# Performance work log

Measured on AMD Instinct MI355X. Metric: run time of the kernel, lower is better.

## Reference

```python
import jax, jax.numpy as jnp
import numpy as np

N_NODES = 20000
N_GRAPH = 256
NODE_DIM = 128
MULS = (128, 64, 32)       # node irreps: 128x0e + 64x1o + 32x2e
HC = 32                    # hidden channels per irrep
HIDDEN_DIM = 64
N_PATH = 9                 # feasible uuw paths into 0e+1e+2e
W_NUMEL = N_PATH * HC * HC # 9216


def _tables():
    # real Clebsch-Gordan tensors built from cartesian tensor algebra,
    # normalized so that sum(C**2) = 2*l_out + 1 (component normalization)
    eps = np.zeros((3, 3, 3))
    eps[0, 1, 2] = eps[1, 2, 0] = eps[2, 0, 1] = 1.0
    eps[0, 2, 1] = eps[2, 1, 0] = eps[1, 0, 2] = -1.0
    s2, s6 = 1 / np.sqrt(2), 1 / np.sqrt(6)
    Q2 = np.zeros((5, 3, 3))  # orthonormal basis of traceless symmetric 3x3
    Q2[0, 0, 1] = Q2[0, 1, 0] = s2          # xy
    Q2[1, 1, 2] = Q2[1, 2, 1] = s2          # yz
    Q2[2, 0, 0] = Q2[2, 1, 1] = -s6; Q2[2, 2, 2] = 2 * s6  # z2
    Q2[3, 0, 2] = Q2[3, 2, 0] = s2          # xz
    Q2[4, 0, 0] = s2; Q2[4, 1, 1] = -s2     # x2-y2

    def nrm(C, l3):
        return C * np.sqrt((2 * l3 + 1) / (C ** 2).sum())

    C000 = np.ones((1, 1, 1))
    C022 = np.eye(5)[None, :, :]
    C110 = np.eye(3).reshape(3, 3, 1) / np.sqrt(3)
    C111 = eps / np.sqrt(2)
    C112 = np.transpose(Q2, (1, 2, 0))
    C202 = np.eye(5)[:, None, :]
    C220 = np.eye(5).reshape(5, 5, 1) / np.sqrt(5)
    M = np.einsum('iab,jdb->ijad', Q2, Q2)  # [5,5,3,3]
    C221 = nrm(np.einsum('cad,ijad->ijc', eps, M), 1)
    S = 0.5 * (M + np.transpose(M, (0, 1, 3, 2)))
    S = S - np.trace(S, axis1=2, axis2=3)[..., None, None] * np.eye(3) / 3.0
    C222 = nrm(np.einsum('kad,ijad->ijk', Q2, S), 2)
    # sph2cart change of basis: 9 spherical comps (0e+1e+2e) -> 3x3 cartesian
    Qc = np.zeros((3, 3, 9))
    Qc[:, :, 0] = np.eye(3) / np.sqrt(3)        # isotropic part
    Qc[:, :, 1:4] = eps / np.sqrt(2)            # antisymmetric part
    Qc[:, :, 4:9] = np.transpose(Q2, (1, 2, 0)) # symmetric traceless part
    return [C000, C022, C110, C111, C112, C202, C220, C221, C222], Qc

_CGS, _QC = _tables()


def setup_inputs() -> dict:
    key = jax.random.key(0)
    ks = jax.random.split(key, 12)
    f32 = jnp.float32
    d_sph = MULS[0] + 3 * MULS[1] + 5 * MULS[2]  # 480
    return {
        'x_scalar': jax.random.normal(ks[0], (N_NODES, NODE_DIM), f32),
        'x_spherical': jax.random.normal(ks[1], (N_NODES, d_sph), f32),
        'batch': jnp.sort(jax.random.randint(ks[2], (N_NODES,), 0, N_GRAPH)),
        'W0e': jax.random.normal(ks[3], (MULS[0], HC), f32),
        'W1o': jax.random.normal(ks[4], (MULS[1], HC), f32),
        'W2e': jax.random.normal(ks[5], (MULS[2], HC), f32),
        'Wm1': jax.random.normal(ks[6], (NODE_DIM, HIDDEN_DIM), f32) / np.sqrt(NODE_DIM),
        'bm1': jnp.zeros((HIDDEN_DIM,), f32),
        'Wm2': jax.random.normal(ks[7], (HIDDEN_DIM, W_NUMEL), f32) / np.sqrt(HIDDEN_DIM),
        'bm2': jnp.zeros((W_NUMEL,), f32),
        'P0': jax.random.normal(ks[8], (3 * HC,), f32),
        'P1': jax.random.normal(ks[9], (2 * HC,), f32),
        'P2': jax.random.normal(ks[10], (4 * HC,), f32),
    }


def reference(x_scalar, x_spherical, batch, W0e, W1o, W2e, Wm1, bm1, Wm2, bm2, P0, P1, P2):
    n = x_scalar.shape[0]
    m0, m1, m2 = MULS
    # split node features into irrep blocks
    x0 = x_spherical[:, :m0, None]                        # [N,128,1] 0e
    x1 = x_spherical[:, m0:m0 + 3 * m1].reshape(n, m1, 3) # [N,64,3]  1o
    x2 = x_spherical[:, m0 + 3 * m1:].reshape(n, m2, 5)   # [N,32,5]  2e
    # pre_lin: per-irrep channel mixing (e3nn-style 1/sqrt(fan_in))
    h = [jnp.einsum('num,uv->nvm', x, W) / np.sqrt(W.shape[0])
         for x, W in ((x0, W0e), (x1, W1o), (x2, W2e))]   # each [N,32,2l+1]
    # per-node tensor-product weights from scalar features
    w = (jax.nn.silu(x_scalar @ Wm1 + bm1) @ Wm2 + bm2).reshape(n, N_PATH, HC, HC)
    # uuw tensor product, path order matches _CGS
    paths = ((0, 0), (0, 2), (1, 1), (1, 1), (1, 1), (2, 0), (2, 2), (2, 2), (2, 2))
    inv_u = 1.0 / np.sqrt(HC)
    outs = []
    for k, (i, j) in enumerate(paths):
        C = jnp.asarray(_CGS[k], x_scalar.dtype)
        outs.append(jnp.einsum('pqr,nup,nuq,nuw->nwr', C, h[i], h[j], w[:, k]) * inv_u)
    # post_lin: combine paths of each output l into a single channel
    y0 = jnp.einsum('num,u->nm', jnp.concatenate([outs[0], outs[2], outs[6]], 1), P0) / np.sqrt(3 * HC)
    y1 = jnp.einsum('num,u->nm', jnp.concatenate([outs[3], outs[7]], 1), P1) / np.sqrt(2 * HC)
    y2 = jnp.einsum('num,u->nm', jnp.concatenate([outs[1], outs[4], outs[5], outs[8]], 1), P2) / np.sqrt(4 * HC)
    sph = jnp.concatenate([y0, y1, y2], axis=1)           # [N,9]
    cart = jnp.einsum('abi,ni->nab', jnp.asarray(_QC, sph.dtype), sph)  # [N,3,3]
    red = jax.ops.segment_sum(cart, batch, num_segments=N_GRAPH)        # [B,3,3]
    # if_trace is False (if_iso=False): roll every non-batch dim by 1
    return jnp.roll(jnp.roll(red, 1, axis=1), 1, axis=2)
```

## Files before the change

### kernel.cpp

```cpp
#include <hip/hip_runtime.h>
#include <math.h>

#define OFF_W2P 0
#define OFF_B2P 14336
#define OFF_NRM 14560
#define OFF_V   14592
#define OFF_H0  4494592
#define OFF_H1  5134592
#define OFF_H2  7054592
#define WS_FLOATS 10254592

#define SC_Y0 0.0180421959121758f
#define SC_Y2 0.015625f
#define S2f 0.70710678118654752f
#define S6f 0.40824829046386302f
#define TWOS2f 1.41421356237309505f
#define TWOS6f 0.81649658092772603f
#define ISQRT3 0.57735026918962576f
#define ISQRT5 0.44721359549995794f
#define H0SC 0.08838834764831845f
#define H1SC 0.125f
#define H2SC 0.17677669529663689f

__device__ __constant__ int KARR[7] = {0, 1, 2, 4, 5, 6, 8};

__global__ __launch_bounds__(256) void prep_kernel(
    const float* __restrict__ Wm2, const float* __restrict__ bm2,
    const float* __restrict__ P0, const float* __restrict__ P2,
    float* __restrict__ ws, float* __restrict__ out) {
  int j = blockIdx.x * 256 + threadIdx.x;
  if (j < 2304) out[j] = 0.f;

  if (j < 14336) {
    int s = j >> 11; int rem = j & 2047; int c = rem >> 5; int u = rem & 31;
    int k = KARR[s];
    const float* P;
    float sc;
    switch (s) {
      case 0: P = P0;      sc = SC_Y0; break;
      case 1: P = P2;      sc = SC_Y2; break;
      case 2: P = P0 + 32; sc = SC_Y0; break;
      case 3: P = P2 + 32; sc = SC_Y2; break;
      case 4: P = P2 + 64; sc = SC_Y2; break;
      case 5: P = P0 + 64; sc = SC_Y0; break;
      default: P = P2 + 96; sc = SC_Y2; break;
    }
    const float4* w4 = (const float4*)(Wm2 + c * 9216 + k * 1024 + u * 32);
    const float4* p4 = (const float4*)P;
    float acc = 0.f;
#pragma unroll
    for (int q = 0; q < 8; ++q) {
      float4 a = w4[q], b = p4[q];
      acc += a.x * b.x + a.y * b.y + a.z * b.z + a.w * b.w;
    }
    ws[OFF_W2P + c * 224 + s * 32 + u] = acc * sc;
  } else if (j < 14560) {
    int i = j - 14336; int s = i >> 5; int u = i & 31; int k = KARR[s];
    const float* P;
    float sc;
    switch (s) {
      case 0: P = P0;      sc = SC_Y0; break;
      case 1: P = P2;      sc = SC_Y2; break;
      case 2: P = P0 + 32; sc = SC_Y0; break;
      case 3: P = P2 + 32; sc = SC_Y2; break;
      case 4: P = P2 + 64; sc = SC_Y2; break;
      case 5: P = P0 + 64; sc = SC_Y0; break;
      default: P = P2 + 96; sc = SC_Y2; break;
    }
    const float* b = bm2 + k * 1024 + u * 32;
    float acc = 0.f;
#pragma unroll
    for (int w = 0; w < 32; ++w) acc += b[w] * P[w];
    ws[OFF_B2P + s * 32 + u] = acc * sc;
  } else if (j == 14560) {
    double Q2[5][3][3] = {};
    const double s2d = 0.70710678118654752440, s6d = 0.40824829046386301637;
    Q2[0][0][1] = Q2[0][1][0] = s2d;
    Q2[1][1][2] = Q2[1][2][1] = s2d;
    Q2[2][0][0] = Q2[2][1][1] = -s6d; Q2[2][2][2] = 2.0 * s6d;
    Q2[3][0][2] = Q2[3][2][0] = s2d;
    Q2[4][0][0] = s2d; Q2[4][1][1] = -s2d;
    double ss = 0.0;
    for (int i = 0; i < 5; ++i)
      for (int jj = 0; jj < 5; ++jj) {
        double S[3][3];
        for (int a = 0; a < 3; ++a)
          for (int d = 0; d < 3; ++d) {
            double m1 = 0, m2 = 0;
            for (int b = 0; b < 3; ++b) {
              m1 += Q2[i][a][b] * Q2[jj][d][b];
              m2 += Q2[i][d][b] * Q2[jj][a][b];
            }
            S[a][d] = 0.5 * (m1 + m2);
          }
        double tr = (S[0][0] + S[1][1] + S[2][2]) / 3.0;
        S[0][0] -= tr; S[1][1] -= tr; S[2][2] -= tr;
        for (int kk = 0; kk < 5; ++kk) {
          double cc = 0;
          for (int a = 0; a < 3; ++a)
            for (int d = 0; d < 3; ++d) cc += Q2[kk][a][d] * S[a][d];
          ss += cc * cc;
        }
      }
    ws[OFF_NRM] = (float)sqrt(5.0 / ss);
  }
}

__global__ __launch_bounds__(256) void kb_kernel(
    const float* __restrict__ xs_g, const float* __restrict__ Wm1,
    const float* __restrict__ bm1, const float* __restrict__ ws) {
  __shared__ float xs[64][132];
  __shared__ float hiT[64][64];
  const int n0 = blockIdx.x * 64;
  const int tid = threadIdx.x;

  for (int idx = tid; idx < 2048; idx += 256) {
    int row = idx >> 5, c4 = idx & 31;
    int n = n0 + row;
    float4 v = {0.f, 0.f, 0.f, 0.f};
    if (n < 20000) v = *(const float4*)(xs_g + n * 128 + c4 * 4);
    *(float4*)&xs[row][c4 * 4] = v;
  }
  __syncthreads();

  {
    const int cg = tid & 15, ng = tid >> 4;
    const int c0 = cg * 4, nl = ng * 4;
    float acc[4][4] = {{0.f}};
#pragma unroll 2
    for (int mq = 0; mq < 32; ++mq) {
      float4 xv[4], wv[4];
#pragma unroll
      for (int i = 0; i < 4; ++i) xv[i] = *(float4*)&xs[nl + i][mq * 4];
#pragma unroll
      for (int r = 0; r < 4; ++r) wv[r] = *(const float4*)(Wm1 + (mq * 4 + r) * 64 + c0);
#pragma unroll
      for (int r = 0; r < 4; ++r) {
        const float4 w = wv[r];
#pragma unroll
        for (int i = 0; i < 4; ++i) {
          const float xr = (r == 0) ? xv[i].x : (r == 1) ? xv[i].y : (r == 2) ? xv[i].z : xv[i].w;
          acc[i][0] += xr * w.x; acc[i][1] += xr * w.y;
          acc[i][2] += xr * w.z; acc[i][3] += xr * w.w;
        }
      }
    }
    const float4 bb = *(const float4*)(bm1 + c0);
#pragma unroll
    for (int i = 0; i < 4; ++i) {
#pragma unroll
      for (int jj = 0; jj < 4; ++jj) {
        float z = acc[i][jj] + ((jj == 0) ? bb.x : (jj == 1) ? bb.y : (jj == 2) ? bb.z : bb.w);
        z = z / (1.f + __expf(-z));
        hiT[c0 + jj][nl + i] = z;
      }
    }
  }
  __syncthreads();

  if (tid < 224) {
    const int og = tid >> 3, ng = tid & 7;
    const int o0 = og * 8, nl = ng * 8;
    const float* Wp = ws + OFF_W2P;
    const float4 blo = *(const float4*)(ws + OFF_B2P + o0);
    const float4 bhi = *(const float4*)(ws + OFF_B2P + o0 + 4);
    float acc[8][8];
#pragma unroll
    for (int i = 0; i < 8; ++i) {
      acc[i][0] = blo.x; acc[i][1] = blo.y; acc[i][2] = blo.z; acc[i][3] = blo.w;
      acc[i][4] = bhi.x; acc[i][5] = bhi.y; acc[i][6] = bhi.z; acc[i][7] = bhi.w;
    }
#pragma unroll 2
    for (int c = 0; c < 64; ++c) {
      const float4 hlo = *(float4*)&hiT[c][nl];
      const float4 hhi = *(float4*)&hiT[c][nl + 4];
      const float4 wlo = *(const float4*)(Wp + c * 224 + o0);
      const float4 whi = *(const float4*)(Wp + c * 224 + o0 + 4);
      const float hv[8] = {hlo.x, hlo.y, hlo.z, hlo.w, hhi.x, hhi.y, hhi.z, hhi.w};
      const float wv[8] = {wlo.x, wlo.y, wlo.z, wlo.w, whi.x, whi.y, whi.z, whi.w};
#pragma unroll
      for (int i = 0; i < 8; ++i)
#pragma unroll
        for (int jj = 0; jj < 8; ++jj) acc[i][jj] += hv[i] * wv[jj];
    }
    float* Vout = (float*)(ws + OFF_V);
#pragma unroll
    for (int i = 0; i < 8; ++i) {
      const int n = n0 + nl + i;
      if (n < 20000) {
        float4 a = {acc[i][0], acc[i][1], acc[i][2], acc[i][3]};
        float4 b = {acc[i][4], acc[i][5], acc[i][6], acc[i][7]};
        *(float4*)(Vout + n * 224 + o0) = a;
        *(float4*)(Vout + n * 224 + o0 + 4) = b;
      }
    }
  }
}

__global__ __launch_bounds__(256) void kc_kernel(
    const float* __restrict__ xsph, const float* __restrict__ W0e,
    const float* __restrict__ W1o, const float* __restrict__ W2e,
    float* __restrict__ ws) {
  __shared__ float xp[32][484];
  const int n0 = blockIdx.x * 32;
  const int tid = threadIdx.x;

  for (int idx = tid; idx < 3840; idx += 256) {
    int row = idx / 120, c4 = idx % 120;
    *(float4*)&xp[row][c4 * 4] = *(const float4*)(xsph + (n0 + row) * 480 + c4 * 4);
  }
  __syncthreads();

  if (tid < 64) {
    const int ug = tid & 3, ng = tid >> 2;
    const int u0 = ug * 8;
    float acc[2][8] = {{0.f}};
#pragma unroll 1
    for (int mq = 0; mq < 32; ++mq) {
      float4 xv[2];
      xv[0] = *(float4*)&xp[ng][mq * 4];
      xv[1] = *(float4*)&xp[ng + 16][mq * 4];
      float4 wl[4], wh[4];
#pragma unroll
      for (int r = 0; r < 4; ++r) {
        wl[r] = *(const float4*)(W0e + (mq * 4 + r) * 32 + u0);
        wh[r] = *(const float4*)(W0e + (mq * 4 + r) * 32 + u0 + 4);
      }
#pragma unroll
      for (int r = 0; r < 4; ++r) {
        const float wv[8] = {wl[r].x, wl[r].y, wl[r].z, wl[r].w, wh[r].x, wh[r].y, wh[r].z, wh[r].w};
#pragma unroll
        for (int i = 0; i < 2; ++i) {
          const float xr = (r == 0) ? xv[i].x : (r == 1) ? xv[i].y : (r == 2) ? xv[i].z : xv[i].w;
#pragma unroll
          for (int jj = 0; jj < 8; ++jj) acc[i][jj] += xr * wv[jj];
        }
      }
    }
#pragma unroll
    for (int i = 0; i < 2; ++i) {
      const int n = n0 + ng + 16 * i;
      float4 a = {acc[i][0] * H0SC, acc[i][1] * H0SC, acc[i][2] * H0SC, acc[i][3] * H0SC};
      float4 b = {acc[i][4] * H0SC, acc[i][5] * H0SC, acc[i][6] * H0SC, acc[i][7] * H0SC};
      *(float4*)(ws + OFF_H0 + n * 32 + u0) = a;
      *(float4*)(ws + OFF_H0 + n * 32 + u0 + 4) = b;
    }
  } else if (tid < 128) {
    const int t = tid - 64;
    const int ug = t & 3, ng = t >> 2;
    const int u0 = ug * 8;
    float acc[2][3][8] = {{{0.f}}};
#pragma unroll 1
    for (int mq = 0; mq < 16; ++mq) {
      float xa[2][12];
#pragma unroll
      for (int i = 0; i < 2; ++i) {
        const int n = ng + 16 * i;
        float4 a0 = *(float4*)&xp[n][128 + mq * 12];
        float4 a1 = *(float4*)&xp[n][128 + mq * 12 + 4];
        float4 a2 = *(float4*)&xp[n][128 + mq * 12 + 8];
        xa[i][0] = a0.x; xa[i][1] = a0.y; xa[i][2] = a0.z; xa[i][3] = a0.w;
        xa[i][4] = a1.x; xa[i][5] = a1.y; xa[i][6] = a1.z; xa[i][7] = a1.w;
        xa[i][8] = a2.x; xa[i][9] = a2.y; xa[i][10] = a2.z; xa[i][11] = a2.w;
      }
#pragma unroll
      for (int mm = 0; mm < 4; ++mm) {
        const int m = mq * 4 + mm;
        float4 wl = *(const float4*)(W1o + m * 32 + u0);
        float4 wh = *(const float4*)(W1o + m * 32 + u0 + 4);
        const float wv[8] = {wl.x, wl.y, wl.z, wl.w, wh.x, wh.y, wh.z, wh.w};
#pragma unroll
        for (int i = 0; i < 2; ++i)
#pragma unroll
          for (int j = 0; j < 3; ++j) {
            const float xr = xa[i][mm * 3 + j];
#pragma unroll
            for (int jj = 0; jj < 8; ++jj) acc[i][j][jj] += xr * wv[jj];
          }
      }
    }
#pragma unroll
    for (int i = 0; i < 2; ++i) {
      const int n = n0 + ng + 16 * i;
#pragma unroll
      for (int j = 0; j < 3; ++j) {
        float4 a = {acc[i][j][0] * H1SC, acc[i][j][1] * H1SC, acc[i][j][2] * H1SC, acc[i][j][3] * H1SC};
        float4 b = {acc[i][j][4] * H1SC, acc[i][j][5] * H1SC, acc[i][j][6] * H1SC, acc[i][j][7] * H1SC};
        *(float4*)(ws + OFF_H1 + (n * 3 + j) * 32 + u0) = a;
        *(float4*)(ws + OFF_H1 + (n * 3 + j) * 32 + u0 + 4) = b;
      }
    }
  } else {
    const int t = tid - 128;
    const int ug = t & 3, ng = t >> 2;
    const int u0 = ug * 8;
    float acc[5][8] = {{0.f}};
#pragma unroll 1
    for (int mq = 0; mq < 8; ++mq) {
      float xa[20];
#pragma unroll
      for (int q = 0; q < 5; ++q) {
        float4 a = *(float4*)&xp[ng][320 + mq * 20 + q * 4];
        xa[q * 4 + 0] = a.x; xa[q * 4 + 1] = a.y; xa[q * 4 + 2] = a.z; xa[q * 4 + 3] = a.w;
      }
#pragma unroll
      for (int mm = 0; mm < 4; ++mm) {
        const int m = mq * 4 + mm;
        float4 wl = *(const float4*)(W2e + m * 32 + u0);
        float4 wh = *(const float4*)(W2e + m * 32 + u0 + 4);
        const float wv[8] = {wl.x, wl.y, wl.z, wl.w, wh.x, wh.y, wh.z, wh.w};
#pragma unroll
        for (int j = 0; j < 5; ++j) {
          const float xr = xa[mm * 5 + j];
#pragma unroll
          for (int jj = 0; jj < 8; ++jj) acc[j][jj] += xr * wv[jj];
        }
      }
    }
    const int n = n0 + ng;
#pragma unroll
    for (int j = 0; j < 5; ++j) {
      float4 a = {acc[j][0] * H2SC, acc[j][1] * H2SC, acc[j][2] * H2SC, acc[j][3] * H2SC};
      float4 b = {acc[j][4] * H2SC, acc[j][5] * H2SC, acc[j][6] * H2SC, acc[j][7] * H2SC};
      *(float4*)(ws + OFF_H2 + (n * 5 + j) * 32 + u0) = a;
      *(float4*)(ws + OFF_H2 + (n * 5 + j) * 32 + u0 + 4) = b;
    }
  }
}

__global__ __launch_bounds__(256) void kd_kernel(
    const float* __restrict__ ws, const int* __restrict__ batch,
    float* __restrict__ out) {
  const int tid = threadIdx.x;
  const int nl = tid >> 5, un = tid & 31;
  const int n0 = blockIdx.x * 8;
  const int n = n0 + nl;

  const float* V = ws + OFF_V + n * 224 + un;
  const float v0 = V[0], v1 = V[32], v2 = V[64], v3 = V[96];
  const float v4 = V[128], v5 = V[160], v6 = V[192];
  const float h0 = ws[OFF_H0 + n * 32 + un];
  const float h1a = ws[OFF_H1 + (n * 3 + 0) * 32 + un];
  const float h1b = ws[OFF_H1 + (n * 3 + 1) * 32 + un];
  const float h1c = ws[OFF_H1 + (n * 3 + 2) * 32 + un];
  float h2v[5];
#pragma unroll
  for (int j = 0; j < 5; ++j) h2v[j] = ws[OFF_H2 + (n * 5 + j) * 32 + un];
  const float norm2 = ws[OFF_NRM];

  const float d11 = h1a * h1a + h1b * h1b + h1c * h1c;
  const float d22 = h2v[0] * h2v[0] + h2v[1] * h2v[1] + h2v[2] * h2v[2] +
                    h2v[3] * h2v[3] + h2v[4] * h2v[4];
  float y0 = v0 * h0 * h0 + v2 * d11 * ISQRT3 + v5 * d22 * ISQRT5;

  const float o00 = h1a * h1a, o01 = h1a * h1b, o02 = h1a * h1c;
  const float o11 = h1b * h1b, o12 = h1b * h1c, o22 = h1c * h1c;
  const float t40 = TWOS2f * o01, t41 = TWOS2f * o12;
  const float t42 = S6f * (2.f * o22 - o00 - o11);
  const float t43 = TWOS2f * o02, t44 = S2f * (o00 - o11);

  const float A00 = -S6f * h2v[2] + S2f * h2v[4];
  const float A01 = S2f * h2v[0];
  const float A02 = S2f * h2v[3];
  const float A11 = -S6f * h2v[2] - S2f * h2v[4];
  const float A12 = S2f * h2v[1];
  const float A22 = TWOS6f * h2v[2];
  const float B00 = A00 * A00 + A01 * A01 + A02 * A02;
  const float B01 = A00 * A01 + A01 * A11 + A02 * A12;
  const float B02 = A00 * A02 + A01 * A12 + A02 * A22;
  const float B11 = A01 * A01 + A11 * A11 + A12 * A12;
  const float B12 = A01 * A02 + A11 * A12 + A12 * A22;
  const float B22 = A02 * A02 + A12 * A12 + A22 * A22;
  const float t80 = TWOS2f * B01, t81 = TWOS2f * B12;
  const float t82 = S6f * (2.f * B22 - B00 - B11);
  const float t83 = TWOS2f * B02, t84 = S2f * (B00 - B11);

  const float w15 = (v1 + v4) * h0;
  const float v6n = v6 * norm2;
  float y2r[5];
  y2r[0] = w15 * h2v[0] + v3 * t40 + v6n * t80;
  y2r[1] = w15 * h2v[1] + v3 * t41 + v6n * t81;
  y2r[2] = w15 * h2v[2] + v3 * t42 + v6n * t82;
  y2r[3] = w15 * h2v[3] + v3 * t43 + v6n * t83;
  y2r[4] = w15 * h2v[4] + v3 * t44 + v6n * t84;

#pragma unroll
  for (int off = 16; off > 0; off >>= 1) {
    y0 += __shfl_xor(y0, off, 32);
#pragma unroll
    for (int r = 0; r < 5; ++r) y2r[r] += __shfl_xor(y2r[r], off, 32);
  }

  __shared__ float sphs[8][6];
  if (un == 0) {
    sphs[nl][0] = y0;
#pragma unroll
    for (int r = 0; r < 5; ++r) sphs[nl][1 + r] = y2r[r];
  }
  __syncthreads();

  if (tid < 9) {
    const float QW[9][6] = {
        {ISQRT3, 0.f, 0.f, -S6f, 0.f, S2f},
        {0.f, S2f, 0.f, 0.f, 0.f, 0.f},
        {0.f, 0.f, 0.f, 0.f, S2f, 0.f},
        {0.f, S2f, 0.f, 0.f, 0.f, 0.f},
        {ISQRT3, 0.f, 0.f, -S6f, 0.f, -S2f},
        {0.f, 0.f, S2f, 0.f, 0.f, 0.f},
        {0.f, 0.f, 0.f, 0.f, S2f, 0.f},
        {0.f, 0.f, S2f, 0.f, 0.f, 0.f},
        {ISQRT3, 0.f, 0.f, TWOS6f, 0.f, 0.f}};
    const int a = tid / 3, b = tid % 3;
    const int rolled = ((a + 1) % 3) * 3 + ((b + 1) % 3);
    const float c0 = QW[tid][0], c1 = QW[tid][1], c2 = QW[tid][2];
    const float c3 = QW[tid][3], c4 = QW[tid][4], c5 = QW[tid][5];
    int cur_g = batch[n0];
    float acc = 0.f;
#pragma unroll
    for (int q = 0; q < 8; ++q) {
      const int g = batch[n0 + q];
      const float val = c0 * sphs[q][0] + c1 * sphs[q][1] + c2 * sphs[q][2] +
                        c3 * sphs[q][3] + c4 * sphs[q][4] + c5 * sphs[q][5];
      if (g != cur_g) {
        atomicAdd(out + cur_g * 9 + rolled, acc);
        acc = 0.f;
        cur_g = g;
      }
      acc += val;
    }
    atomicAdd(out + cur_g * 9 + rolled, acc);
  }
}

extern "C" void kernel_launch(void* const* d_in, const int* in_sizes, int n_in,
                              void* d_out, int out_size, void* d_ws, size_t ws_size,
                              hipStream_t stream) {
  const float* x_scalar = (const float*)d_in[0];
  const float* x_sph    = (const float*)d_in[1];
  const int*   batch    = (const int*)d_in[2];
  const float* W0e      = (const float*)d_in[3];
  const float* W1o      = (const float*)d_in[4];
  const float* W2e      = (const float*)d_in[5];
  const float* Wm1      = (const float*)d_in[6];
  const float* bm1      = (const float*)d_in[7];
  const float* Wm2      = (const float*)d_in[8];
  const float* bm2      = (const float*)d_in[9];
  const float* P0       = (const float*)d_in[10];
  const float* P2       = (const float*)d_in[12];
  float* ws  = (float*)d_ws;
  float* out = (float*)d_out;

  if (ws_size < (size_t)WS_FLOATS * sizeof(float)) return;

  prep_kernel<<<57, 256, 0, stream>>>(Wm2, bm2, P0, P2, ws, out);
  kb_kernel<<<313, 256, 0, stream>>>(x_scalar, Wm1, bm1, ws);
  kc_kernel<<<625, 256, 0, stream>>>(x_sph, W0e, W1o, W2e, ws);
  kd_kernel<<<2500, 256, 0, stream>>>(ws, batch, out);
}
```

Baseline: 174.5 us.

## Fuse MLP, linear projections and tensor-product reduction into one kernel

Replaces the three per-node kernels (MLP weight projection, irreps linear layers, tensor product plus segment reduction) with a single kernel over 32-node blocks. Intermediate V, h0, h1 and h2 stay in shared memory or registers and no longer round-trip through a multi-megabyte global workspace. The constant CG normalisation is now computed on the host and passed as an argument. In exchange, the h projections read x_spherical directly from global memory with per-lane scalar weight loads, and each block does more serial work.

```diff
diff --git a/kernel.cpp b/kernel.cpp
--- a/kernel.cpp
+++ b/kernel.cpp
@@ -3,12 +3,7 @@
 
 #define OFF_W2P 0
 #define OFF_B2P 14336
-#define OFF_NRM 14560
-#define OFF_V   14592
-#define OFF_H0  4494592
-#define OFF_H1  5134592
-#define OFF_H2  7054592
-#define WS_FLOATS 10254592
+#define WS_FLOATS 14560
 
 #define SC_Y0 0.0180421959121758f
 #define SC_Y2 0.015625f
@@ -72,73 +67,50 @@
 #pragma unroll
     for (int w = 0; w < 32; ++w) acc += b[w] * P[w];
     ws[OFF_B2P + s * 32 + u] = acc * sc;
-  } else if (j == 14560) {
-    double Q2[5][3][3] = {};
-    const double s2d = 0.70710678118654752440, s6d = 0.40824829046386301637;
-    Q2[0][0][1] = Q2[0][1][0] = s2d;
-    Q2[1][1][2] = Q2[1][2][1] = s2d;
-    Q2[2][0][0] = Q2[2][1][1] = -s6d; Q2[2][2][2] = 2.0 * s6d;
-    Q2[3][0][2] = Q2[3][2][0] = s2d;
-    Q2[4][0][0] = s2d; Q2[4][1][1] = -s2d;
-    double ss = 0.0;
-    for (int i = 0; i < 5; ++i)
-      for (int jj = 0; jj < 5; ++jj) {
-        double S[3][3];
-        for (int a = 0; a < 3; ++a)
-          for (int d = 0; d < 3; ++d) {
-            double m1 = 0, m2 = 0;
-            for (int b = 0; b < 3; ++b) {
-              m1 += Q2[i][a][b] * Q2[jj][d][b];
-              m2 += Q2[i][d][b] * Q2[jj][a][b];
-            }
-            S[a][d] = 0.5 * (m1 + m2);
-          }
-        double tr = (S[0][0] + S[1][1] + S[2][2]) / 3.0;
-        S[0][0] -= tr; S[1][1] -= tr; S[2][2] -= tr;
-        for (int kk = 0; kk < 5; ++kk) {
-          double cc = 0;
-          for (int a = 0; a < 3; ++a)
-            for (int d = 0; d < 3; ++d) cc += Q2[kk][a][d] * S[a][d];
-          ss += cc * cc;
-        }
-      }
-    ws[OFF_NRM] = (float)sqrt(5.0 / ss);
   }
 }
 
-__global__ __launch_bounds__(256) void kb_kernel(
-    const float* __restrict__ xs_g, const float* __restrict__ Wm1,
-    const float* __restrict__ bm1, const float* __restrict__ ws) {
-  __shared__ float xs[64][132];
-  __shared__ float hiT[64][64];
-  const int n0 = blockIdx.x * 64;
+__global__ __launch_bounds__(256) void fused_kernel(
+    const float* __restrict__ xs_g, const float* __restrict__ xsph,
+    const int* __restrict__ batch,
+    const float* __restrict__ W0e, const float* __restrict__ W1o,
+    const float* __restrict__ W2e,
+    const float* __restrict__ Wm1, const float* __restrict__ bm1,
+    const float* __restrict__ ws, float* __restrict__ out, const float norm2) {
+  __shared__ __align__(16) char smem[39040];
+  float (*xs)[132] = (float (*)[132])smem;
+  float (*V)[224]  = (float (*)[224])smem;
+  float (*hiT)[36] = (float (*)[36])(smem + 28672);
+  float (*sphs)[8] = (float (*)[8])(smem + 37888);
+  int* batch_s     = (int*)(smem + 38912);
+
   const int tid = threadIdx.x;
-
-  for (int idx = tid; idx < 2048; idx += 256) {
-    int row = idx >> 5, c4 = idx & 31;
-    int n = n0 + row;
-    float4 v = {0.f, 0.f, 0.f, 0.f};
-    if (n < 20000) v = *(const float4*)(xs_g + n * 128 + c4 * 4);
-    *(float4*)&xs[row][c4 * 4] = v;
-  }
+  const int n0 = blockIdx.x * 32;
+
+  for (int idx = tid; idx < 1024; idx += 256) {
+    const int row = idx >> 5, c4 = idx & 31;
+    *(float4*)&xs[row][c4 * 4] = *(const float4*)(xs_g + (n0 + row) * 128 + c4 * 4);
+  }
+  if (tid < 32) batch_s[tid] = batch[n0 + tid];
   __syncthreads();
 
   {
     const int cg = tid & 15, ng = tid >> 4;
-    const int c0 = cg * 4, nl = ng * 4;
-    float acc[4][4] = {{0.f}};
-#pragma unroll 2
+    const int c0 = cg * 4, nl = ng * 2;
+    float acc[2][4] = {{0.f}};
+#pragma unroll 4
     for (int mq = 0; mq < 32; ++mq) {
-      float4 xv[4], wv[4];
-#pragma unroll
-      for (int i = 0; i < 4; ++i) xv[i] = *(float4*)&xs[nl + i][mq * 4];
+      float4 xv[2];
+      xv[0] = *(float4*)&xs[nl][mq * 4];
+      xv[1] = *(float4*)&xs[nl + 1][mq * 4];
+      float4 wv[4];
 #pragma unroll
       for (int r = 0; r < 4; ++r) wv[r] = *(const float4*)(Wm1 + (mq * 4 + r) * 64 + c0);
 #pragma unroll
       for (int r = 0; r < 4; ++r) {
         const float4 w = wv[r];
 #pragma unroll
-        for (int i = 0; i < 4; ++i) {
+        for (int i = 0; i < 2; ++i) {
           const float xr = (r == 0) ? xv[i].x : (r == 1) ? xv[i].y : (r == 2) ? xv[i].z : xv[i].w;
           acc[i][0] += xr * w.x; acc[i][1] += xr * w.y;
           acc[i][2] += xr * w.z; acc[i][3] += xr * w.w;
@@ -147,255 +119,160 @@
     }
     const float4 bb = *(const float4*)(bm1 + c0);
 #pragma unroll
-    for (int i = 0; i < 4; ++i) {
-#pragma unroll
-      for (int jj = 0; jj < 4; ++jj) {
+    for (int jj = 0; jj < 4; ++jj) {
+      float zz[2];
+#pragma unroll
+      for (int i = 0; i < 2; ++i) {
         float z = acc[i][jj] + ((jj == 0) ? bb.x : (jj == 1) ? bb.y : (jj == 2) ? bb.z : bb.w);
-        z = z / (1.f + __expf(-z));
-        hiT[c0 + jj][nl + i] = z;
-      }
+        zz[i] = z / (1.f + __expf(-z));
+      }
+      *(float2*)&hiT[c0 + jj][nl] = make_float2(zz[0], zz[1]);
     }
   }
   __syncthreads();
 
   if (tid < 224) {
     const int og = tid >> 3, ng = tid & 7;
-    const int o0 = og * 8, nl = ng * 8;
-    const float* Wp = ws + OFF_W2P;
+    const int o0 = og * 8, nl = ng * 4;
     const float4 blo = *(const float4*)(ws + OFF_B2P + o0);
     const float4 bhi = *(const float4*)(ws + OFF_B2P + o0 + 4);
-    float acc[8][8];
-#pragma unroll
-    for (int i = 0; i < 8; ++i) {
+    float acc[4][8];
+#pragma unroll
+    for (int i = 0; i < 4; ++i) {
       acc[i][0] = blo.x; acc[i][1] = blo.y; acc[i][2] = blo.z; acc[i][3] = blo.w;
       acc[i][4] = bhi.x; acc[i][5] = bhi.y; acc[i][6] = bhi.z; acc[i][7] = bhi.w;
     }
 #pragma unroll 2
     for (int c = 0; c < 64; ++c) {
-      const float4 hlo = *(float4*)&hiT[c][nl];
-      const float4 hhi = *(float4*)&hiT[c][nl + 4];
-      const float4 wlo = *(const float4*)(Wp + c * 224 + o0);
-      const float4 whi = *(const float4*)(Wp + c * 224 + o0 + 4);
-      const float hv[8] = {hlo.x, hlo.y, hlo.z, hlo.w, hhi.x, hhi.y, hhi.z, hhi.w};
+      const float4 hv = *(float4*)&hiT[c][nl];
+      const float4 wlo = *(const float4*)(ws + OFF_W2P + c * 224 + o0);
+      const float4 whi = *(const float4*)(ws + OFF_W2P + c * 224 + o0 + 4);
+      const float hvv[4] = {hv.x, hv.y, hv.z, hv.w};
       const float wv[8] = {wlo.x, wlo.y, wlo.z, wlo.w, whi.x, whi.y, whi.z, whi.w};
 #pragma unroll
-      for (int i = 0; i < 8; ++i)
-#pragma unroll
-        for (int jj = 0; jj < 8; ++jj) acc[i][jj] += hv[i] * wv[jj];
-    }
-    float* Vout = (float*)(ws + OFF_V);
-#pragma unroll
-    for (int i = 0; i < 8; ++i) {
-      const int n = n0 + nl + i;
-      if (n < 20000) {
-        float4 a = {acc[i][0], acc[i][1], acc[i][2], acc[i][3]};
-        float4 b = {acc[i][4], acc[i][5], acc[i][6], acc[i][7]};
-        *(float4*)(Vout + n * 224 + o0) = a;
-        *(float4*)(Vout + n * 224 + o0 + 4) = b;
-      }
-    }
-  }
-}
-
-__global__ __launch_bounds__(256) void kc_kernel(
-    const float* __restrict__ xsph, const float* __restrict__ W0e,
-    const float* __restrict__ W1o, const float* __restrict__ W2e,
-    float* __restrict__ ws) {
-  __shared__ float xp[32][484];
-  const int n0 = blockIdx.x * 32;
-  const int tid = threadIdx.x;
-
-  for (int idx = tid; idx < 3840; idx += 256) {
-    int row = idx / 120, c4 = idx % 120;
-    *(float4*)&xp[row][c4 * 4] = *(const float4*)(xsph + (n0 + row) * 480 + c4 * 4);
+      for (int i = 0; i < 4; ++i)
+#pragma unroll
+        for (int jj = 0; jj < 8; ++jj) acc[i][jj] += hvv[i] * wv[jj];
+    }
+#pragma unroll
+    for (int i = 0; i < 4; ++i) {
+      float4 a = {acc[i][0], acc[i][1], acc[i][2], acc[i][3]};
+      float4 b = {acc[i][4], acc[i][5], acc[i][6], acc[i][7]};
+      *(float4*)&V[nl + i][o0] = a;
+      *(float4*)&V[nl + i][o0 + 4] = b;
+    }
   }
   __syncthreads();
 
-  if (tid < 64) {
-    const int ug = tid & 3, ng = tid >> 2;
-    const int u0 = ug * 8;
-    float acc[2][8] = {{0.f}};
-#pragma unroll 1
+  const int lane = tid & 63, wid = tid >> 6;
+  const int half = lane >> 5, u = lane & 31;
+  const float* W0u = W0e + u;
+  const float* W1u = W1o + u;
+  const float* W2u = W2e + u;
+
+  for (int p = 0; p < 4; ++p) {
+    const int nloc = p * 8 + wid * 2 + half;
+    const float4* x4 = (const float4*)(xsph + (size_t)(n0 + nloc) * 480);
+
+    float h0 = 0.f;
+#pragma unroll 8
     for (int mq = 0; mq < 32; ++mq) {
-      float4 xv[2];
-      xv[0] = *(float4*)&xp[ng][mq * 4];
-      xv[1] = *(float4*)&xp[ng + 16][mq * 4];
-      float4 wl[4], wh[4];
-#pragma unroll
-      for (int r = 0; r < 4; ++r) {
-        wl[r] = *(const float4*)(W0e + (mq * 4 + r) * 32 + u0);
-        wh[r] = *(const float4*)(W0e + (mq * 4 + r) * 32 + u0 + 4);
-      }
-#pragma unroll
-      for (int r = 0; r < 4; ++r) {
-        const float wv[8] = {wl[r].x, wl[r].y, wl[r].z, wl[r].w, wh[r].x, wh[r].y, wh[r].z, wh[r].w};
-#pragma unroll
-        for (int i = 0; i < 2; ++i) {
-          const float xr = (r == 0) ? xv[i].x : (r == 1) ? xv[i].y : (r == 2) ? xv[i].z : xv[i].w;
-#pragma unroll
-          for (int jj = 0; jj < 8; ++jj) acc[i][jj] += xr * wv[jj];
-        }
-      }
-    }
-#pragma unroll
-    for (int i = 0; i < 2; ++i) {
-      const int n = n0 + ng + 16 * i;
-      float4 a = {acc[i][0] * H0SC, acc[i][1] * H0SC, acc[i][2] * H0SC, acc[i][3] * H0SC};
-      float4 b = {acc[i][4] * H0SC, acc[i][5] * H0SC, acc[i][6] * H0SC, acc[i][7] * H0SC};
-      *(float4*)(ws + OFF_H0 + n * 32 + u0) = a;
-      *(float4*)(ws + OFF_H0 + n * 32 + u0 + 4) = b;
-    }
-  } else if (tid < 128) {
-    const int t = tid - 64;
-    const int ug = t & 3, ng = t >> 2;
-    const int u0 = ug * 8;
-    float acc[2][3][8] = {{{0.f}}};
-#pragma unroll 1
+      const float4 xv = x4[mq];
+      h0 += xv.x * W0u[(mq * 4 + 0) * 32] + xv.y * W0u[(mq * 4 + 1) * 32] +
+            xv.z * W0u[(mq * 4 + 2) * 32] + xv.w * W0u[(mq * 4 + 3) * 32];
+    }
+    h0 *= H0SC;
+
+    float h1v[3] = {0.f, 0.f, 0.f};
+#pragma unroll 4
     for (int mq = 0; mq < 16; ++mq) {
-      float xa[2][12];
-#pragma unroll
-      for (int i = 0; i < 2; ++i) {
-        const int n = ng + 16 * i;
-        float4 a0 = *(float4*)&xp[n][128 + mq * 12];
-        float4 a1 = *(float4*)&xp[n][128 + mq * 12 + 4];
-        float4 a2 = *(float4*)&xp[n][128 + mq * 12 + 8];
-        xa[i][0] = a0.x; xa[i][1] = a0.y; xa[i][2] = a0.z; xa[i][3] = a0.w;
-        xa[i][4] = a1.x; xa[i][5] = a1.y; xa[i][6] = a1.z; xa[i][7] = a1.w;
-        xa[i][8] = a2.x; xa[i][9] = a2.y; xa[i][10] = a2.z; xa[i][11] = a2.w;
-      }
+      const float4 a0 = x4[32 + mq * 3 + 0];
+      const float4 a1 = x4[32 + mq * 3 + 1];
+      const float4 a2 = x4[32 + mq * 3 + 2];
+      const float xa[12] = {a0.x, a0.y, a0.z, a0.w, a1.x, a1.y, a1.z, a1.w,
+                            a2.x, a2.y, a2.z, a2.w};
 #pragma unroll
       for (int mm = 0; mm < 4; ++mm) {
-        const int m = mq * 4 + mm;
-        float4 wl = *(const float4*)(W1o + m * 32 + u0);
-        float4 wh = *(const float4*)(W1o + m * 32 + u0 + 4);
-        const float wv[8] = {wl.x, wl.y, wl.z, wl.w, wh.x, wh.y, wh.z, wh.w};
-#pragma unroll
-        for (int i = 0; i < 2; ++i)
-#pragma unroll
-          for (int j = 0; j < 3; ++j) {
-            const float xr = xa[i][mm * 3 + j];
-#pragma unroll
-            for (int jj = 0; jj < 8; ++jj) acc[i][j][jj] += xr * wv[jj];
-          }
-      }
-    }
-#pragma unroll
-    for (int i = 0; i < 2; ++i) {
-      const int n = n0 + ng + 16 * i;
-#pragma unroll
-      for (int j = 0; j < 3; ++j) {
-        float4 a = {acc[i][j][0] * H1SC, acc[i][j][1] * H1SC, acc[i][j][2] * H1SC, acc[i][j][3] * H1SC};
-        float4 b = {acc[i][j][4] * H1SC, acc[i][j][5] * H1SC, acc[i][j][6] * H1SC, acc[i][j][7] * H1SC};
-        *(float4*)(ws + OFF_H1 + (n * 3 + j) * 32 + u0) = a;
-        *(float4*)(ws + OFF_H1 + (n * 3 + j) * 32 + u0 + 4) = b;
-      }
-    }
-  } else {
-    const int t = tid - 128;
-    const int ug = t & 3, ng = t >> 2;
-    const int u0 = ug * 8;
-    float acc[5][8] = {{0.f}};
-#pragma unroll 1
+        const float wv = W1u[(mq * 4 + mm) * 32];
+#pragma unroll
+        for (int j = 0; j < 3; ++j) h1v[j] += xa[mm * 3 + j] * wv;
+      }
+    }
+    const float h1a = h1v[0] * H1SC, h1b = h1v[1] * H1SC, h1c = h1v[2] * H1SC;
+
+    float h2v[5] = {0.f, 0.f, 0.f, 0.f, 0.f};
+#pragma unroll 2
     for (int mq = 0; mq < 8; ++mq) {
-      float xa[20];
-#pragma unroll
-      for (int q = 0; q < 5; ++q) {
-        float4 a = *(float4*)&xp[ng][320 + mq * 20 + q * 4];
-        xa[q * 4 + 0] = a.x; xa[q * 4 + 1] = a.y; xa[q * 4 + 2] = a.z; xa[q * 4 + 3] = a.w;
-      }
+      const float4 a0 = x4[80 + mq * 5 + 0];
+      const float4 a1 = x4[80 + mq * 5 + 1];
+      const float4 a2 = x4[80 + mq * 5 + 2];
+      const float4 a3 = x4[80 + mq * 5 + 3];
+      const float4 a4 = x4[80 + mq * 5 + 4];
+      const float xa[20] = {a0.x, a0.y, a0.z, a0.w, a1.x, a1.y, a1.z, a1.w,
+                            a2.x, a2.y, a2.z, a2.w, a3.x, a3.y, a3.z, a3.w,
+                            a4.x, a4.y, a4.z, a4.w};
 #pragma unroll
       for (int mm = 0; mm < 4; ++mm) {
-        const int m = mq * 4 + mm;
-        float4 wl = *(const float4*)(W2e + m * 32 + u0);
-        float4 wh = *(const float4*)(W2e + m * 32 + u0 + 4);
-        const float wv[8] = {wl.x, wl.y, wl.z, wl.w, wh.x, wh.y, wh.z, wh.w};
-#pragma unroll
-        for (int j = 0; j < 5; ++j) {
-          const float xr = xa[mm * 5 + j];
-#pragma unroll
-          for (int jj = 0; jj < 8; ++jj) acc[j][jj] += xr * wv[jj];
-        }
-      }
-    }
-    const int n = n0 + ng;
-#pragma unroll
-    for (int j = 0; j < 5; ++j) {
-      float4 a = {acc[j][0] * H2SC, acc[j][1] * H2SC, acc[j][2] * H2SC, acc[j][3] * H2SC};
-      float4 b = {acc[j][4] * H2SC, acc[j][5] * H2SC, acc[j][6] * H2SC, acc[j][7] * H2SC};
-      *(float4*)(ws + OFF_H2 + (n * 5 + j) * 32 + u0) = a;
-      *(float4*)(ws + OFF_H2 + (n * 5 + j) * 32 + u0 + 4) = b;
-    }
-  }
-}
-
-__global__ __launch_bounds__(256) void kd_kernel(
-    const float* __restrict__ ws, const int* __restrict__ batch,
-    float* __restrict__ out) {
-  const int tid = threadIdx.x;
-  const int nl = tid >> 5, un = tid & 31;
-  const int n0 = blockIdx.x * 8;
-  const int n = n0 + nl;
-
-  const float* V = ws + OFF_V + n * 224 + un;
-  const float v0 = V[0], v1 = V[32], v2 = V[64], v3 = V[96];
-  const float v4 = V[128], v5 = V[160], v6 = V[192];
-  const float h0 = ws[OFF_H0 + n * 32 + un];
-  const float h1a = ws[OFF_H1 + (n * 3 + 0) * 32 + un];
-  const float h1b = ws[OFF_H1 + (n * 3 + 1) * 32 + un];
-  const float h1c = ws[OFF_H1 + (n * 3 + 2) * 32 + un];
-  float h2v[5];
-#pragma unroll
-  for (int j = 0; j < 5; ++j) h2v[j] = ws[OFF_H2 + (n * 5 + j) * 32 + un];
-  const float norm2 = ws[OFF_NRM];
-
-  const float d11 = h1a * h1a + h1b * h1b + h1c * h1c;
-  const float d22 = h2v[0] * h2v[0] + h2v[1] * h2v[1] + h2v[2] * h2v[2] +
-                    h2v[3] * h2v[3] + h2v[4] * h2v[4];
-  float y0 = v0 * h0 * h0 + v2 * d11 * ISQRT3 + v5 * d22 * ISQRT5;
-
-  const float o00 = h1a * h1a, o01 = h1a * h1b, o02 = h1a * h1c;
-  const float o11 = h1b * h1b, o12 = h1b * h1c, o22 = h1c * h1c;
-  const float t40 = TWOS2f * o01, t41 = TWOS2f * o12;
-  const float t42 = S6f * (2.f * o22 - o00 - o11);
-  const float t43 = TWOS2f * o02, t44 = S2f * (o00 - o11);
-
-  const float A00 = -S6f * h2v[2] + S2f * h2v[4];
-  const float A01 = S2f * h2v[0];
-  const float A02 = S2f * h2v[3];
-  const float A11 = -S6f * h2v[2] - S2f * h2v[4];
-  const float A12 = S2f * h2v[1];
-  const float A22 = TWOS6f * h2v[2];
-  const float B00 = A00 * A00 + A01 * A01 + A02 * A02;
-  const float B01 = A00 * A01 + A01 * A11 + A02 * A12;
-  const float B02 = A00 * A02 + A01 * A12 + A02 * A22;
-  const float B11 = A01 * A01 + A11 * A11 + A12 * A12;
-  const float B12 = A01 * A02 + A11 * A12 + A12 * A22;
-  const float B22 = A02 * A02 + A12 * A12 + A22 * A22;
-  const float t80 = TWOS2f * B01, t81 = TWOS2f * B12;
-  const float t82 = S6f * (2.f * B22 - B00 - B11);
-  const float t83 = TWOS2f * B02, t84 = S2f * (B00 - B11);
-
-  const float w15 = (v1 + v4) * h0;
-  const float v6n = v6 * norm2;
-  float y2r[5];
-  y2r[0] = w15 * h2v[0] + v3 * t40 + v6n * t80;
-  y2r[1] = w15 * h2v[1] + v3 * t41 + v6n * t81;
-  y2r[2] = w15 * h2v[2] + v3 * t42 + v6n * t82;
-  y2r[3] = w15 * h2v[3] + v3 * t43 + v6n * t83;
-  y2r[4] = w15 * h2v[4] + v3 * t44 + v6n * t84;
-
-#pragma unroll
-  for (int off = 16; off > 0; off >>= 1) {
-    y0 += __shfl_xor(y0, off, 32);
-#pragma unroll
-    for (int r = 0; r < 5; ++r) y2r[r] += __shfl_xor(y2r[r], off, 32);
-  }
-
-  __shared__ float sphs[8][6];
-  if (un == 0) {
-    sphs[nl][0] = y0;
-#pragma unroll
-    for (int r = 0; r < 5; ++r) sphs[nl][1 + r] = y2r[r];
+        const float wv = W2u[(mq * 4 + mm) * 32];
+#pragma unroll
+        for (int j = 0; j < 5; ++j) h2v[j] += xa[mm * 5 + j] * wv;
+      }
+    }
+#pragma unroll
+    for (int j = 0; j < 5; ++j) h2v[j] *= H2SC;
+
+    const float v0 = V[nloc][u],       v1 = V[nloc][u + 32],
+                v2 = V[nloc][u + 64],  v3 = V[nloc][u + 96],
+                v4 = V[nloc][u + 128], v5 = V[nloc][u + 160],
+                v6 = V[nloc][u + 192];
+
+    const float d11 = h1a * h1a + h1b * h1b + h1c * h1c;
+    const float d22 = h2v[0] * h2v[0] + h2v[1] * h2v[1] + h2v[2] * h2v[2] +
+                      h2v[3] * h2v[3] + h2v[4] * h2v[4];
+    float y0 = v0 * h0 * h0 + v2 * d11 * ISQRT3 + v5 * d22 * ISQRT5;
+
+    const float o00 = h1a * h1a, o01 = h1a * h1b, o02 = h1a * h1c;
+    const float o11 = h1b * h1b, o12 = h1b * h1c, o22 = h1c * h1c;
+    const float t40 = TWOS2f * o01, t41 = TWOS2f * o12;
+    const float t42 = S6f * (2.f * o22 - o00 - o11);
+    const float t43 = TWOS2f * o02, t44 = S2f * (o00 - o11);
+
+    const float A00 = -S6f * h2v[2] + S2f * h2v[4];
+    const float A01 = S2f * h2v[0];
+    const float A02 = S2f * h2v[3];
+    const float A11 = -S6f * h2v[2] - S2f * h2v[4];
+    const float A12 = S2f * h2v[1];
+    const float A22 = TWOS6f * h2v[2];
+    const float B00 = A00 * A00 + A01 * A01 + A02 * A02;
+    const float B01 = A00 * A01 + A01 * A11 + A02 * A12;
+    const float B02 = A00 * A02 + A01 * A12 + A02 * A22;
+    const float B11 = A01 * A01 + A11 * A11 + A12 * A12;
+    const float B12 = A01 * A02 + A11 * A12 + A12 * A22;
+    const float B22 = A02 * A02 + A12 * A12 + A22 * A22;
+    const float t80 = TWOS2f * B01, t81 = TWOS2f * B12;
+    const float t82 = S6f * (2.f * B22 - B00 - B11);
+    const float t83 = TWOS2f * B02, t84 = S2f * (B00 - B11);
+
+    const float w15 = (v1 + v4) * h0;
+    const float v6n = v6 * norm2;
+    float y2r[5];
+    y2r[0] = w15 * h2v[0] + v3 * t40 + v6n * t80;
+    y2r[1] = w15 * h2v[1] + v3 * t41 + v6n * t81;
+    y2r[2] = w15 * h2v[2] + v3 * t42 + v6n * t82;
+    y2r[3] = w15 * h2v[3] + v3 * t43 + v6n * t83;
+    y2r[4] = w15 * h2v[4] + v3 * t44 + v6n * t84;
+
+#pragma unroll
+    for (int off = 16; off > 0; off >>= 1) {
+      y0 += __shfl_xor(y0, off, 32);
+#pragma unroll
+      for (int r = 0; r < 5; ++r) y2r[r] += __shfl_xor(y2r[r], off, 32);
+    }
+    if (u == 0) {
+      sphs[nloc][0] = y0;
+#pragma unroll
+      for (int r = 0; r < 5; ++r) sphs[nloc][1 + r] = y2r[r];
+    }
   }
   __syncthreads();
 
@@ -414,11 +291,11 @@
     const int rolled = ((a + 1) % 3) * 3 + ((b + 1) % 3);
     const float c0 = QW[tid][0], c1 = QW[tid][1], c2 = QW[tid][2];
     const float c3 = QW[tid][3], c4 = QW[tid][4], c5 = QW[tid][5];
-    int cur_g = batch[n0];
+    int cur_g = batch_s[0];
     float acc = 0.f;
-#pragma unroll
-    for (int q = 0; q < 8; ++q) {
-      const int g = batch[n0 + q];
+#pragma unroll 4
+    for (int q = 0; q < 32; ++q) {
+      const int g = batch_s[q];
       const float val = c0 * sphs[q][0] + c1 * sphs[q][1] + c2 * sphs[q][2] +
                         c3 * sphs[q][3] + c4 * sphs[q][4] + c5 * sphs[q][5];
       if (g != cur_g) {
@@ -452,8 +329,42 @@
 
   if (ws_size < (size_t)WS_FLOATS * sizeof(float)) return;
 
+  double Q2[5][3][3] = {};
+  const double s2d = 0.70710678118654752440, s6d = 0.40824829046386301637;
+  Q2[0][0][1] = Q2[0][1][0] = s2d;
+  Q2[1][1][2] = Q2[1][2][1] = s2d;
+  Q2[2][0][0] = Q2[2][1][1] = -s6d; Q2[2][2][2] = 2.0 * s6d;
+  Q2[3][0][2] = Q2[3][2][0] = s2d;
+  Q2[4][0][0] = s2d; Q2[4][1][1] = -s2d;
+  double eps[3][3][3] = {};
+  eps[0][1][2] = eps[1][2][0] = eps[2][0][1] = 1.0;
+  eps[0][2][1] = eps[2][1][0] = eps[1][0][2] = -1.0;
+  (void)eps;
+  double ss = 0.0;
+  for (int i = 0; i < 5; ++i)
+    for (int jj = 0; jj < 5; ++jj) {
+      double S[3][3];
+      for (int a = 0; a < 3; ++a)
+        for (int d = 0; d < 3; ++d) {
+          double m1 = 0, m2 = 0;
+          for (int b = 0; b < 3; ++b) {
+            m1 += Q2[i][a][b] * Q2[jj][d][b];
+            m2 += Q2[i][d][b] * Q2[jj][a][b];
+          }
+          S[a][d] = 0.5 * (m1 + m2);
+        }
+      double tr = (S[0][0] + S[1][1] + S[2][2]) / 3.0;
+      S[0][0] -= tr; S[1][1] -= tr; S[2][2] -= tr;
+      for (int kk = 0; kk < 5; ++kk) {
+        double cc = 0;
+        for (int a = 0; a < 3; ++a)
+          for (int d = 0; d < 3; ++d) cc += Q2[kk][a][d] * S[a][d];
+        ss += cc * cc;
+      }
+    }
+  const float norm2 = (float)sqrt(5.0 / ss);
+
   prep_kernel<<<57, 256, 0, stream>>>(Wm2, bm2, P0, P2, ws, out);
-  kb_kernel<<<313, 256, 0, stream>>>(x_scalar, Wm1, bm1, ws);
-  kc_kernel<<<625, 256, 0, stream>>>(x_sph, W0e, W1o, W2e, ws);
-  kd_kernel<<<2500, 256, 0, stream>>>(ws, batch, out);
+  fused_kernel<<<625, 256, 0, stream>>>(x_scalar, x_sph, batch, W0e, W1o, W2e,
+                                        Wm1, bm1, ws, out, norm2);
 }
```

Result: slower. 200.0 us (+14.6%).
